# Performance work log

Measured on AMD Instinct MI355X. Metric: run time of the kernel, lower is better.

Reference implementation:

```python
import jax, jax.numpy as jnp
import numpy as np

K_BITS = 4
V_BITS = 4
GROUP_SIZE = 64
EPS = 1e-8


def _quant_dequant_per_token(x, bits):
    # TurboQuantProd: symmetric per-token (per head_dim vector) absmax quantization.
    qmax = 2.0 ** (bits - 1) - 1.0
    scale = jnp.maximum(jnp.max(jnp.abs(x), axis=-1, keepdims=True) / qmax, EPS)
    return jnp.clip(jnp.round(x / scale), -qmax, qmax) * scale


def _quant_dequant_grouped(x, bits, group_size):
    # TurboQuantValue: symmetric grouped absmax quantization along head_dim.
    shp = x.shape
    xg = x.reshape(shp[:-1] + (shp[-1] // group_size, group_size))
    qmax = 2.0 ** (bits - 1) - 1.0
    scale = jnp.maximum(jnp.max(jnp.abs(xg), axis=-1, keepdims=True) / qmax, EPS)
    dq = jnp.clip(jnp.round(xg / scale), -qmax, qmax) * scale
    return dq.reshape(shp)


def setup_inputs() -> dict:
    key = jax.random.key(0)
    kq, kk, kv = jax.random.split(key, 3)
    B, H, S, D = 2, 16, 2048, 128
    query = jax.random.normal(kq, (B, H, S, D), dtype=jnp.float32)
    k = jax.random.normal(kk, (B, H, S, D), dtype=jnp.float32)
    v = jax.random.normal(kv, (B, H, S, D), dtype=jnp.float32)
    causal_mask = jnp.tril(jnp.ones((S, S), dtype=bool))[None, None]  # [1,1,S,S]
    return {"query": query, "key": k, "value": v, "causal_mask": causal_mask}


def reference(query, key, value, causal_mask):
    # Non-protected path: quantize K per-token, V grouped, then fused dequant + SDPA.
    head_dim = query.shape[-1]
    scale = 1.0 / np.sqrt(head_dim).astype(np.float32)
    dq_key = _quant_dequant_per_token(key, K_BITS)
    dq_value = _quant_dequant_grouped(value, V_BITS, GROUP_SIZE)
    scores = jnp.einsum('bhqd,bhkd->bhqk', query, dq_key) * scale
    scores = jnp.where(causal_mask, scores, -jnp.inf)
    weights = jax.nn.softmax(scores, axis=-1)
    output = jnp.einsum('bhqk,bhkd->bhqd', weights, dq_value)
    return (output, weights)
```

## Files before the change

kernel.cpp:

```cpp
#include <hip/hip_runtime.h>

#define SQ 2048
#define DD 128
#define BHN 32
#define SC2 0.12751741934f

typedef __attribute__((ext_vector_type(8))) short bf16x8;
typedef __attribute__((ext_vector_type(4))) float f32x4;

__device__ __forceinline__ unsigned short f2bf(float x){
  unsigned int u = __float_as_uint(x);
  unsigned int r = (u + 0x7FFFu + ((u >> 16) & 1u)) >> 16;
  return (unsigned short)r;
}
__device__ __forceinline__ unsigned pack2bf(float a, float b){
  return (unsigned)f2bf(a) | ((unsigned)f2bf(b) << 16);
}

__device__ __forceinline__ void gl_lds16(const void* g, void* l){
  __builtin_amdgcn_global_load_lds(
      (const __attribute__((address_space(1))) unsigned int*)g,
      (__attribute__((address_space(3))) unsigned int*)l, 16, 0, 0);
}

__global__ __launch_bounds__(256) void qd_kernel(const float* __restrict__ K,
                                                 const float* __restrict__ V,
                                                 char* __restrict__ dqK,
                                                 char* __restrict__ dqVt){
  __shared__ float Vlds[128*65];
  const int t = threadIdx.x;
  const int bh = blockIdx.x >> 5;
  const int stile = blockIdx.x & 31;
  const int tt = t >> 2;
  const int q4 = t & 3;
  const int s = stile*64 + tt;
  const long ebase = ((long)(bh*SQ + s))*DD + 32*q4;

  float vals[32];
  {
    const float4* kp = (const float4*)(K + ebase);
    float am = 0.f;
    #pragma unroll
    for (int j=0;j<8;j++){
      float4 v4 = kp[j];
      vals[4*j+0]=v4.x; vals[4*j+1]=v4.y; vals[4*j+2]=v4.z; vals[4*j+3]=v4.w;
      am = fmaxf(am, fmaxf(fmaxf(fabsf(v4.x),fabsf(v4.y)),fmaxf(fabsf(v4.z),fabsf(v4.w))));
    }
    am = fmaxf(am, __shfl_xor(am,1));
    am = fmaxf(am, __shfl_xor(am,2));
    const float sc = fmaxf(am/7.0f, 1e-8f);
    #pragma unroll
    for (int j=0;j<32;j++){
      float qv = rintf(vals[j]/sc);
      qv = fminf(7.f, fmaxf(-7.f, qv));
      vals[j] = qv*sc;
    }
    const long rowb = ((long)(bh*SQ + s))*256;
    const int swz = (s & 7) << 4;
    #pragma unroll
    for (int c=0;c<4;c++){
      uint4 w;
      w.x = pack2bf(vals[8*c+0], vals[8*c+1]);
      w.y = pack2bf(vals[8*c+2], vals[8*c+3]);
      w.z = pack2bf(vals[8*c+4], vals[8*c+5]);
      w.w = pack2bf(vals[8*c+6], vals[8*c+7]);
      *(uint4*)(dqK + rowb + ((64*q4 + 16*c) ^ swz)) = w;
    }
  }
  {
    const float4* vp = (const float4*)(V + ebase);
    float am = 0.f;
    #pragma unroll
    for (int j=0;j<8;j++){
      float4 v4 = vp[j];
      vals[4*j+0]=v4.x; vals[4*j+1]=v4.y; vals[4*j+2]=v4.z; vals[4*j+3]=v4.w;
      am = fmaxf(am, fmaxf(fmaxf(fabsf(v4.x),fabsf(v4.y)),fmaxf(fabsf(v4.z),fabsf(v4.w))));
    }
    am = fmaxf(am, __shfl_xor(am,1));
    const float sc = fmaxf(am/7.0f, 1e-8f);
    #pragma unroll
    for (int j=0;j<32;j++){
      float qv = rintf(vals[j]/sc);
      qv = fminf(7.f, fmaxf(-7.f, qv));
      Vlds[(32*q4 + j)*65 + tt] = qv*sc;
    }
  }
  __syncthreads();
  #pragma unroll
  for (int m=0;m<4;m++){
    const int chunk = m*256 + t;
    const int d = chunk >> 3;
    const int c = chunk & 7;
    uint4 w;
    const float* f = &Vlds[d*65 + 8*c];
    w.x = pack2bf(f[0], f[1]);
    w.y = pack2bf(f[2], f[3]);
    w.z = pack2bf(f[4], f[5]);
    w.w = pack2bf(f[6], f[7]);
    const long ob = ((long)(bh*DD + d))*4096 + (long)stile*128 + ((16*c) ^ ((d&7)<<4));
    *(uint4*)(dqVt + ob) = w;
  }
}

__global__ __launch_bounds__(256,2) void attn_fused(const float* __restrict__ Q,
    const char* __restrict__ dqK, const char* __restrict__ dqVt,
    float* __restrict__ Out, float* __restrict__ Wout){
  __shared__ __attribute__((aligned(16))) char Kt[2][16384];
  __shared__ __attribute__((aligned(16))) char Vt[2][16384];
  __shared__ __attribute__((aligned(16))) char Et[4][4096];

  const int bid = blockIdx.x;
  const int xcd = bid & 7;
  const int loc = bid >> 3;
  const int bh  = xcd*4 + (loc & 3);
  const int p   = loc >> 2;
  const int t = threadIdx.x;
  const int lane = t & 63;
  const int w = t >> 6;
  const int s = w >> 1;
  const int ws = w & 1;
  const int l15 = lane & 15, l4 = lane >> 4;
  const int swz = (l15 & 7) << 4;

  const int qt   = s ? p : (31 - p);
  const int q0   = qt * 64;
  const int nktA = 32 - p;
  const int myNkt = qt + 1;
  const int rbase = q0 + 32*ws;

  bf16x8 qa[2][4];
  #pragma unroll
  for (int g=0; g<2; ++g){
    const float* qb = Q + ((long)(bh*SQ) + rbase + 16*g + l15)*DD + 8*l4;
    #pragma unroll
    for (int kk=0;kk<4;kk++){
      float4 a = *(const float4*)(qb + 32*kk);
      float4 b = *(const float4*)(qb + 32*kk + 4);
      bf16x8 r;
      r[0]=(short)f2bf(a.x); r[1]=(short)f2bf(a.y); r[2]=(short)f2bf(a.z); r[3]=(short)f2bf(a.w);
      r[4]=(short)f2bf(b.x); r[5]=(short)f2bf(b.y); r[6]=(short)f2bf(b.z); r[7]=(short)f2bf(b.w);
      qa[g][kk]=r;
    }
  }

  const char* Kb = dqK + (long)bh*SQ*256;
  const char* Vb = dqVt + (long)bh*DD*4096;

  const f32x4 z4 = {0.f,0.f,0.f,0.f};
  f32x4 oacc[2][8] = {{z4,z4,z4,z4,z4,z4,z4,z4},{z4,z4,z4,z4,z4,z4,z4,z4}};
  float ssum[2] = {0.f, 0.f};
  char* eb = &Et[w][0];

  auto stageKV = [&](int buf, int kt){
    const char* ks = Kb + (long)kt*16384;
    #pragma unroll
    for (int i=0;i<4;i++)
      gl_lds16(ks + i*4096 + t*16, &Kt[buf][i*4096 + t*16]);
    const char* vs = Vb + (long)kt*128;
    #pragma unroll
    for (int i=0;i<4;i++)
      gl_lds16(vs + (long)(i*32 + (t>>3))*4096 + (t&7)*16, &Vt[buf][i*4096 + t*16]);
  };
  auto stageK = [&](int buf, int kt){
    const char* ks = Kb + (long)kt*16384;
    #pragma unroll
    for (int i=0;i<4;i++)
      gl_lds16(ks + i*4096 + t*16, &Kt[buf][i*4096 + t*16]);
  };

  stageKV(0, 0);
  __syncthreads();
  int cur = 0;
  for (int kt=0; kt<nktA; ++kt){
    if (kt+1 < nktA) stageKV(cur^1, kt+1);

    if (kt < myNkt){
      f32x4 sacc[2][4] = {{z4,z4,z4,z4},{z4,z4,z4,z4}};
      {
        const char* kbase = &Kt[cur][0] + l15*256;
        __builtin_amdgcn_s_setprio(1);
        #pragma unroll
        for (int cf=0;cf<4;cf++){
          #pragma unroll
          for (int kk=0;kk<4;kk++){
            bf16x8 kb = *(const bf16x8*)(kbase + cf*4096 + ((64*kk+16*l4) ^ swz));
            sacc[0][cf] = __builtin_amdgcn_mfma_f32_16x16x32_bf16(kb, qa[0][kk], sacc[0][cf], 0,0,0);
            sacc[1][cf] = __builtin_amdgcn_mfma_f32_16x16x32_bf16(kb, qa[1][kk], sacc[1][cf], 0,0,0);
          }
        }
        __builtin_amdgcn_s_setprio(0);
      }

      const int k0 = kt*64;
      if (kt < qt){
        #pragma unroll
        for (int g=0; g<2; ++g){
          const int lr = 16*g + l15;
          #pragma unroll
          for (int cf=0;cf<4;cf++){
            float e0 = exp2f(sacc[g][cf][0]*SC2);
            float e1 = exp2f(sacc[g][cf][1]*SC2);
            float e2 = exp2f(sacc[g][cf][2]*SC2);
            float e3 = exp2f(sacc[g][cf][3]*SC2);
            ssum[g] += (e0+e1) + (e2+e3);
            uint2 wp; wp.x = pack2bf(e0,e1); wp.y = pack2bf(e2,e3);
            *(uint2*)(eb + lr*128 + ((32*cf + 8*l4) ^ swz)) = wp;
          }
        }
      } else {
        #pragma unroll
        for (int g=0; g<2; ++g){
          const int lr = 16*g + l15;
          const int qrow = rbase + lr;
          #pragma unroll
          for (int cf=0;cf<4;cf++){
            const int tok0 = k0 + 16*cf + 4*l4;
            float e0 = (tok0+0 <= qrow) ? exp2f(sacc[g][cf][0]*SC2) : 0.f;
            float e1 = (tok0+1 <= qrow) ? exp2f(sacc[g][cf][1]*SC2) : 0.f;
            float e2 = (tok0+2 <= qrow) ? exp2f(sacc[g][cf][2]*SC2) : 0.f;
            float e3 = (tok0+3 <= qrow) ? exp2f(sacc[g][cf][3]*SC2) : 0.f;
            ssum[g] += (e0+e1) + (e2+e3);
            uint2 wp; wp.x = pack2bf(e0,e1); wp.y = pack2bf(e2,e3);
            *(uint2*)(eb + lr*128 + ((32*cf + 8*l4) ^ swz)) = wp;
          }
        }
      }

      {
        const char* vbase = &Vt[cur][0] + l15*128;
        __builtin_amdgcn_s_setprio(1);
        #pragma unroll
        for (int kc=0;kc<2;kc++){
          const int eo = (64*kc + 16*l4) ^ swz;
          bf16x8 ea0 = *(const bf16x8*)(eb + l15*128 + eo);
          bf16x8 ea1 = *(const bf16x8*)(eb + (16+l15)*128 + eo);
          #pragma unroll
          for (int df=0;df<8;df++){
            bf16x8 vv = *(const bf16x8*)(vbase + df*2048 + eo);
            oacc[0][df] = __builtin_amdgcn_mfma_f32_16x16x32_bf16(ea0, vv, oacc[0][df], 0,0,0);
            oacc[1][df] = __builtin_amdgcn_mfma_f32_16x16x32_bf16(ea1, vv, oacc[1][df], 0,0,0);
          }
        }
        __builtin_amdgcn_s_setprio(0);
      }
    }
    __syncthreads();
    cur ^= 1;
  }

  float si[2];
  #pragma unroll
  for (int g=0; g<2; ++g){
    float sm = ssum[g];
    sm += __shfl_xor(sm, 16);
    sm += __shfl_xor(sm, 32);
    si[g] = 1.0f / sm;
    float invr[4];
    #pragma unroll
    for (int i=0;i<4;i++) invr[i] = __shfl(si[g], 4*l4+i);
    float* ob = Out + ((long)(bh*SQ) + rbase + 16*g)*DD;
    #pragma unroll
    for (int df=0;df<8;df++){
      #pragma unroll
      for (int i=0;i<4;i++)
        ob[(4*l4+i)*DD + 16*df + l15] = oacc[g][df][i]*invr[i];
    }
  }

  float* Wbase = Wout + (long)bh*SQ*SQ;
  __syncthreads();
  stageK(0, 0);
  __syncthreads();
  cur = 0;
  for (int kt=0; kt<nktA; ++kt){
    if (kt+1 < nktA) stageK(cur^1, kt+1);

    if (kt < myNkt){
      f32x4 sacc[2][4] = {{z4,z4,z4,z4},{z4,z4,z4,z4}};
      {
        const char* kbase = &Kt[cur][0] + l15*256;
        __builtin_amdgcn_s_setprio(1);
        #pragma unroll
        for (int cf=0;cf<4;cf++){
          #pragma unroll
          for (int kk=0;kk<4;kk++){
            bf16x8 kb = *(const bf16x8*)(kbase + cf*4096 + ((64*kk+16*l4) ^ swz));
            sacc[0][cf] = __builtin_amdgcn_mfma_f32_16x16x32_bf16(kb, qa[0][kk], sacc[0][cf], 0,0,0);
            sacc[1][cf] = __builtin_amdgcn_mfma_f32_16x16x32_bf16(kb, qa[1][kk], sacc[1][cf], 0,0,0);
          }
        }
        __builtin_amdgcn_s_setprio(0);
      }
      const int k0 = kt*64;
      if (kt < qt){
        #pragma unroll
        for (int g=0; g<2; ++g){
          float* wrow = Wbase + (long)(rbase + 16*g + l15)*SQ;
          #pragma unroll
          for (int cf=0;cf<4;cf++){
            const int tok0 = k0 + 16*cf + 4*l4;
            float4 wv;
            wv.x = exp2f(sacc[g][cf][0]*SC2)*si[g];
            wv.y = exp2f(sacc[g][cf][1]*SC2)*si[g];
            wv.z = exp2f(sacc[g][cf][2]*SC2)*si[g];
            wv.w = exp2f(sacc[g][cf][3]*SC2)*si[g];
            *(float4*)(wrow + tok0) = wv;
          }
        }
      } else {
        #pragma unroll
        for (int g=0; g<2; ++g){
          const int qrow = rbase + 16*g + l15;
          float* wrow = Wbase + (long)qrow*SQ;
          #pragma unroll
          for (int cf=0;cf<4;cf++){
            const int tok0 = k0 + 16*cf + 4*l4;
            float4 wv;
            wv.x = (tok0+0 <= qrow) ? exp2f(sacc[g][cf][0]*SC2)*si[g] : 0.f;
            wv.y = (tok0+1 <= qrow) ? exp2f(sacc[g][cf][1]*SC2)*si[g] : 0.f;
            wv.z = (tok0+2 <= qrow) ? exp2f(sacc[g][cf][2]*SC2)*si[g] : 0.f;
            wv.w = (tok0+3 <= qrow) ? exp2f(sacc[g][cf][3]*SC2)*si[g] : 0.f;
            *(float4*)(wrow + tok0) = wv;
          }
        }
      }
    }
    __syncthreads();
    cur ^= 1;
  }

  const int z0 = myNkt*64;
  if (z0 < SQ){
    const float4 zz = {0.f,0.f,0.f,0.f};
    for (int rr=0;rr<32;rr++){
      float* row = Wbase + (long)(rbase + rr)*SQ;
      for (int c = z0 + 4*lane; c < SQ; c += 256)
        *(float4*)(row + c) = zz;
    }
  }
}

extern "C" void kernel_launch(void* const* d_in, const int* in_sizes, int n_in,
                              void* d_out, int out_size, void* d_ws, size_t ws_size,
                              hipStream_t stream) {
  const float* Q = (const float*)d_in[0];
  const float* K = (const float*)d_in[1];
  const float* V = (const float*)d_in[2];
  float* Out = (float*)d_out;
  float* Wout = (float*)d_out + (size_t)BHN*SQ*DD;
  char* dqK  = (char*)d_ws;
  char* dqVt = (char*)d_ws + (size_t)BHN*SQ*DD*2;

  qd_kernel<<<BHN*32, 256, 0, stream>>>(K, V, dqK, dqVt);
  attn_fused<<<512, 256, 0, stream>>>(Q, dqK, dqVt, Out, Wout);
}
```

Measured before the change: 242.3 us.

## Read K directly from global in weights pass and use nontemporal weight stores

The second pass, which recomputes scores and writes the normalized attention weights, now loads K fragments straight from global memory into registers per wave. It no longer stages them through LDS with block-wide barriers, so waves iterate only up to their own tile count without synchronizing. The weight matrix and zero-fill writes now use nontemporal stores to avoid polluting cache with the large write-only output. This trades LDS reuse across waves for more global/L2 traffic and higher register use for the K fragments.

```diff
diff --git a/kernel.cpp b/kernel.cpp
--- a/kernel.cpp
+++ b/kernel.cpp
@@ -21,6 +21,10 @@
   __builtin_amdgcn_global_load_lds(
       (const __attribute__((address_space(1))) unsigned int*)g,
       (__attribute__((address_space(3))) unsigned int*)l, 16, 0, 0);
+}
+
+__device__ __forceinline__ void nt_store4(float* p, f32x4 v){
+  __builtin_nontemporal_store(v, (f32x4*)p);
 }
 
 __global__ __launch_bounds__(256) void qd_kernel(const float* __restrict__ K,
@@ -160,12 +164,6 @@
     #pragma unroll
     for (int i=0;i<4;i++)
       gl_lds16(vs + (long)(i*32 + (t>>3))*4096 + (t&7)*16, &Vt[buf][i*4096 + t*16]);
-  };
-  auto stageK = [&](int buf, int kt){
-    const char* ks = Kb + (long)kt*16384;
-    #pragma unroll
-    for (int i=0;i<4;i++)
-      gl_lds16(ks + i*4096 + t*16, &Kt[buf][i*4096 + t*16]);
   };
 
   stageKV(0, 0);
@@ -268,74 +266,77 @@
   }
 
   float* Wbase = Wout + (long)bh*SQ*SQ;
-  __syncthreads();
-  stageK(0, 0);
-  __syncthreads();
-  cur = 0;
-  for (int kt=0; kt<nktA; ++kt){
-    if (kt+1 < nktA) stageK(cur^1, kt+1);
-
-    if (kt < myNkt){
-      f32x4 sacc[2][4] = {{z4,z4,z4,z4},{z4,z4,z4,z4}};
-      {
-        const char* kbase = &Kt[cur][0] + l15*256;
-        __builtin_amdgcn_s_setprio(1);
-        #pragma unroll
-        for (int cf=0;cf<4;cf++){
-          #pragma unroll
-          for (int kk=0;kk<4;kk++){
-            bf16x8 kb = *(const bf16x8*)(kbase + cf*4096 + ((64*kk+16*l4) ^ swz));
-            sacc[0][cf] = __builtin_amdgcn_mfma_f32_16x16x32_bf16(kb, qa[0][kk], sacc[0][cf], 0,0,0);
-            sacc[1][cf] = __builtin_amdgcn_mfma_f32_16x16x32_bf16(kb, qa[1][kk], sacc[1][cf], 0,0,0);
-          }
-        }
-        __builtin_amdgcn_s_setprio(0);
-      }
-      const int k0 = kt*64;
-      if (kt < qt){
-        #pragma unroll
-        for (int g=0; g<2; ++g){
-          float* wrow = Wbase + (long)(rbase + 16*g + l15)*SQ;
-          #pragma unroll
-          for (int cf=0;cf<4;cf++){
-            const int tok0 = k0 + 16*cf + 4*l4;
-            float4 wv;
-            wv.x = exp2f(sacc[g][cf][0]*SC2)*si[g];
-            wv.y = exp2f(sacc[g][cf][1]*SC2)*si[g];
-            wv.z = exp2f(sacc[g][cf][2]*SC2)*si[g];
-            wv.w = exp2f(sacc[g][cf][3]*SC2)*si[g];
-            *(float4*)(wrow + tok0) = wv;
-          }
-        }
-      } else {
-        #pragma unroll
-        for (int g=0; g<2; ++g){
-          const int qrow = rbase + 16*g + l15;
-          float* wrow = Wbase + (long)qrow*SQ;
-          #pragma unroll
-          for (int cf=0;cf<4;cf++){
-            const int tok0 = k0 + 16*cf + 4*l4;
-            float4 wv;
-            wv.x = (tok0+0 <= qrow) ? exp2f(sacc[g][cf][0]*SC2)*si[g] : 0.f;
-            wv.y = (tok0+1 <= qrow) ? exp2f(sacc[g][cf][1]*SC2)*si[g] : 0.f;
-            wv.z = (tok0+2 <= qrow) ? exp2f(sacc[g][cf][2]*SC2)*si[g] : 0.f;
-            wv.w = (tok0+3 <= qrow) ? exp2f(sacc[g][cf][3]*SC2)*si[g] : 0.f;
-            *(float4*)(wrow + tok0) = wv;
-          }
-        }
-      }
-    }
-    __syncthreads();
-    cur ^= 1;
+  float* wrow0 = Wbase + (long)(rbase + l15)*SQ;
+  float* wrow1 = Wbase + (long)(rbase + 16 + l15)*SQ;
+
+  for (int kt=0; kt<myNkt; ++kt){
+    const int k0 = kt*64;
+    const char* kr = Kb + (long)kt*16384 + l15*256;
+
+    bf16x8 kb[4][4];
+    #pragma unroll
+    for (int cf=0;cf<4;cf++){
+      #pragma unroll
+      for (int kk=0;kk<4;kk++)
+        kb[cf][kk] = *(const bf16x8*)(kr + cf*4096 + ((64*kk+16*l4) ^ swz));
+    }
+
+    f32x4 sacc[2][4] = {{z4,z4,z4,z4},{z4,z4,z4,z4}};
+    __builtin_amdgcn_s_setprio(1);
+    #pragma unroll
+    for (int cf=0;cf<4;cf++){
+      #pragma unroll
+      for (int kk=0;kk<4;kk++){
+        sacc[0][cf] = __builtin_amdgcn_mfma_f32_16x16x32_bf16(kb[cf][kk], qa[0][kk], sacc[0][cf], 0,0,0);
+        sacc[1][cf] = __builtin_amdgcn_mfma_f32_16x16x32_bf16(kb[cf][kk], qa[1][kk], sacc[1][cf], 0,0,0);
+      }
+    }
+    __builtin_amdgcn_s_setprio(0);
+
+    if (kt < qt){
+      #pragma unroll
+      for (int cf=0;cf<4;cf++){
+        const int tok0 = k0 + 16*cf + 4*l4;
+        f32x4 wv;
+        wv[0] = exp2f(sacc[0][cf][0]*SC2)*si[0];
+        wv[1] = exp2f(sacc[0][cf][1]*SC2)*si[0];
+        wv[2] = exp2f(sacc[0][cf][2]*SC2)*si[0];
+        wv[3] = exp2f(sacc[0][cf][3]*SC2)*si[0];
+        nt_store4(wrow0 + tok0, wv);
+        wv[0] = exp2f(sacc[1][cf][0]*SC2)*si[1];
+        wv[1] = exp2f(sacc[1][cf][1]*SC2)*si[1];
+        wv[2] = exp2f(sacc[1][cf][2]*SC2)*si[1];
+        wv[3] = exp2f(sacc[1][cf][3]*SC2)*si[1];
+        nt_store4(wrow1 + tok0, wv);
+      }
+    } else {
+      const int qrow0 = rbase + l15;
+      const int qrow1 = rbase + 16 + l15;
+      #pragma unroll
+      for (int cf=0;cf<4;cf++){
+        const int tok0 = k0 + 16*cf + 4*l4;
+        f32x4 wv;
+        wv[0] = (tok0+0 <= qrow0) ? exp2f(sacc[0][cf][0]*SC2)*si[0] : 0.f;
+        wv[1] = (tok0+1 <= qrow0) ? exp2f(sacc[0][cf][1]*SC2)*si[0] : 0.f;
+        wv[2] = (tok0+2 <= qrow0) ? exp2f(sacc[0][cf][2]*SC2)*si[0] : 0.f;
+        wv[3] = (tok0+3 <= qrow0) ? exp2f(sacc[0][cf][3]*SC2)*si[0] : 0.f;
+        nt_store4(wrow0 + tok0, wv);
+        wv[0] = (tok0+0 <= qrow1) ? exp2f(sacc[1][cf][0]*SC2)*si[1] : 0.f;
+        wv[1] = (tok0+1 <= qrow1) ? exp2f(sacc[1][cf][1]*SC2)*si[1] : 0.f;
+        wv[2] = (tok0+2 <= qrow1) ? exp2f(sacc[1][cf][2]*SC2)*si[1] : 0.f;
+        wv[3] = (tok0+3 <= qrow1) ? exp2f(sacc[1][cf][3]*SC2)*si[1] : 0.f;
+        nt_store4(wrow1 + tok0, wv);
+      }
+    }
   }
 
   const int z0 = myNkt*64;
   if (z0 < SQ){
-    const float4 zz = {0.f,0.f,0.f,0.f};
+    const f32x4 zz = {0.f,0.f,0.f,0.f};
     for (int rr=0;rr<32;rr++){
       float* row = Wbase + (long)(rbase + rr)*SQ;
       for (int c = z0 + 4*lane; c < SQ; c += 256)
-        *(float4*)(row + c) = zz;
+        nt_store4(row + c, zz);
     }
   }
 }
```

Measured after the change: 261.9 us. 1.08x slower.
